# Kernel tuning notes

Hardware: AMD Instinct MI355X
Metric: run time of the kernel (lower is better)

The kernel has to match this reference:

```python
import jax, jax.numpy as jnp
import numpy as np

N = 100000   # nodes
E = 1600000  # edges (avg degree 16)
F = 64       # in_feats
H = 128      # hidden_size
O = 10       # out_feats
L = 3        # SAGEConv layers
EPS = 1e-5


def setup_inputs() -> dict:
    key = jax.random.key(0)
    ks = jax.random.split(key, 16)
    s = 0.05
    return {
        "nodes": jax.random.normal(ks[0], (N, F), jnp.float32),
        "src": jax.random.randint(ks[1], (E,), 0, N),
        "dst": jax.random.randint(ks[2], (E,), 0, N),
        # input MLP: Linear(F,H) -> ReLU -> Linear(H,H)
        "W_in1": jax.random.normal(ks[3], (F, H), jnp.float32) * s,
        "b_in1": jnp.zeros((H,), jnp.float32),
        "W_in2": jax.random.normal(ks[4], (H, H), jnp.float32) * s,
        "b_in2": jnp.zeros((H,), jnp.float32),
        # L stacked SAGEConv layers (mean aggregator)
        "W_self": jax.random.normal(ks[5], (L, H, H), jnp.float32) * s,
        "W_neigh": jax.random.normal(ks[6], (L, H, H), jnp.float32) * s,
        "b_sage": jnp.zeros((L, H), jnp.float32),
        "ln_g": jnp.ones((L, H), jnp.float32),
        "ln_b": jnp.zeros((L, H), jnp.float32),
        # output head Linear(H, O)
        "W_out": jax.random.normal(ks[7], (H, O), jnp.float32) * s,
        "b_out": jnp.zeros((O,), jnp.float32),
    }


def reference(nodes, src, dst, W_in1, b_in1, W_in2, b_in2,
              W_self, W_neigh, b_sage, ln_g, ln_b, W_out, b_out):
    # input MLP
    h = jax.nn.relu(nodes @ W_in1 + b_in1) @ W_in2 + b_in2  # [N, H]

    # in-degree for mean aggregation (0-degree nodes get 0 neighbor feature)
    deg = jax.ops.segment_sum(jnp.ones((E,), h.dtype), dst, num_segments=N)
    inv_deg = (1.0 / jnp.maximum(deg, 1.0))[:, None]  # [N, 1]

    for l in range(L):
        # mean over incoming neighbors: gather src feats, scatter-add to dst
        agg = jax.ops.segment_sum(h[src], dst, num_segments=N) * inv_deg  # [N, H]
        h = h @ W_self[l] + agg @ W_neigh[l] + b_sage[l]
        h = jax.nn.relu(h)
        # LayerNorm over feature dim
        mu = h.mean(-1, keepdims=True)
        var = h.var(-1, keepdims=True)
        h = ln_g[l] * (h - mu) * jax.lax.rsqrt(var + EPS) + ln_b[l]

    # dgl.mean_nodes over the single graph -> [1, H]
    g = h.mean(0, keepdims=True)
    return g @ W_out + b_out  # [1, O]
```

## Files before the change

kernel.cpp:

```cpp
#include <hip/hip_runtime.h>
#include <hip/hip_bf16.h>

#define NN 100000
#define NE 1600000
#define FF 64
#define HH 128
#define OO 10
#define NL 3
#define NB 391
#define NBLK 250
#define CHUNK 6400
#define BCAP 5376
#define LNEPS 1e-5f

typedef short s8v __attribute__((ext_vector_type(8)));
typedef float f32x4 __attribute__((ext_vector_type(4)));
typedef float f32x2 __attribute__((ext_vector_type(2)));

__device__ __forceinline__ unsigned short f2b(float f){
  unsigned u = __float_as_uint(f);
  unsigned r = (u + 0x7FFFu + ((u>>16)&1u)) >> 16;
  return (unsigned short)r;
}
__device__ __forceinline__ float b2f(unsigned short b){
  return __uint_as_float(((unsigned)b)<<16);
}

#if __has_builtin(__builtin_amdgcn_cvt_pk_f32_fp8) && __has_builtin(__builtin_amdgcn_cvt_pk_fp8_f32)
__device__ __forceinline__ unsigned char f8enc(float x){
  int p = __builtin_amdgcn_cvt_pk_fp8_f32(x, x, 0, false);
  return (unsigned char)(p & 0xFF);
}
__device__ __forceinline__ void f8dec4(unsigned u, float* o){
  f32x2 lo = __builtin_amdgcn_cvt_pk_f32_fp8(u, false);
  f32x2 hi = __builtin_amdgcn_cvt_pk_f32_fp8(u, true);
  o[0]=lo[0]; o[1]=lo[1]; o[2]=hi[0]; o[3]=hi[1];
}
#else
#include <hip/hip_fp8.h>
__device__ __forceinline__ unsigned char f8enc(float x){
  __hip_fp8_e4m3 q(x); return (unsigned char)q.__x;
}
__device__ __forceinline__ void f8dec4(unsigned u, float* o){
  for(int i=0;i<4;i++){
    __hip_fp8_e4m3 q; q.__x = (unsigned char)(u>>(8*i));
    o[i] = (float)q;
  }
}
#endif

__global__ __launch_bounds__(256) void k_bcount(const int* __restrict__ dst, int* __restrict__ bcnt,
                                                int* __restrict__ blockcnt){
  __shared__ int h[NB];
  for(int i=threadIdx.x;i<NB;i+=256) h[i]=0;
  __syncthreads();
  int base = blockIdx.x*CHUNK;
  for(int i=threadIdx.x;i<CHUNK;i+=256){
    int e = base+i;
    if(e<NE) atomicAdd(&h[((unsigned)dst[e])>>8],1);
  }
  __syncthreads();
  for(int i=threadIdx.x;i<NB;i+=256){
    int v=h[i];
    blockcnt[i*256 + blockIdx.x] = v;
    if(v) atomicAdd(&bcnt[i],v);
  }
}

__global__ void k_bscan(const int* __restrict__ bcnt, int* __restrict__ boff, int* __restrict__ rowoff){
  __shared__ int s[512];
  int t=threadIdx.x;
  int v = (t<NB)? bcnt[t]:0;
  s[t]=v; __syncthreads();
  for(int off=1;off<512;off<<=1){
    int x=(t>=off)?s[t-off]:0;
    __syncthreads();
    s[t]+=x;
    __syncthreads();
  }
  if(t<NB) boff[t]=s[t]-v;
  if(t==0) rowoff[NN]=NE;
}

__global__ void k_prefix(const int* __restrict__ blockcnt, const int* __restrict__ boff,
                         int* __restrict__ pref){
  __shared__ int s[256];
  int k=blockIdx.x, t=threadIdx.x;
  int v = (t<NBLK)? blockcnt[k*256+t] : 0;
  s[t]=v; __syncthreads();
  for(int off=1;off<256;off<<=1){
    int x=(t>=off)?s[t-off]:0;
    __syncthreads();
    s[t]+=x;
    __syncthreads();
  }
  if(t<NBLK) pref[k*256+t] = boff[k] + s[t]-v;
}

__global__ __launch_bounds__(256) void k_bscatter(const int* __restrict__ src, const int* __restrict__ dst,
                                                  const int* __restrict__ pref, unsigned* __restrict__ ebuf){
  __shared__ int cur[NB];
  __shared__ int pb[NB];
  for(int i=threadIdx.x;i<NB;i+=256){ cur[i]=0; pb[i]=pref[i*256+blockIdx.x]; }
  __syncthreads();
  int base=blockIdx.x*CHUNK;
  for(int i=threadIdx.x;i<CHUNK;i+=256){
    int e=base+i;
    if(e<NE){
      int d=dst[e];
      int k=((unsigned)d)>>8;
      int r=atomicAdd(&cur[k],1);
      ebuf[pb[k]+r] = (unsigned)src[e] | ((unsigned)(d&255)<<20);
    }
  }
}

__global__ __launch_bounds__(256) void k_bsort(const unsigned* __restrict__ ebuf, const int* __restrict__ bcnt,
                                               const int* __restrict__ boff, int* __restrict__ rowoff,
                                               float* __restrict__ invd, int* __restrict__ csr){
  __shared__ unsigned el[BCAP];
  __shared__ int dg[256], sc[256], cu[256];
  int b=blockIdx.x, t=threadIdx.x;
  int c = bcnt[b]; if(c>BCAP) c=BCAP;
  int base = boff[b];
  for(int i=t;i<c;i+=256) el[i]=ebuf[base+i];
  dg[t]=0;
  __syncthreads();
  for(int i=t;i<c;i+=256) atomicAdd(&dg[el[i]>>20],1);
  __syncthreads();
  int v = dg[t];
  sc[t]=v; __syncthreads();
  for(int off=1;off<256;off<<=1){
    int x=(t>=off)?sc[t-off]:0;
    __syncthreads();
    sc[t]+=x;
    __syncthreads();
  }
  int excl = sc[t]-v;
  int node = b*256+t;
  if(node<NN){
    rowoff[node]=base+excl;
    invd[node]=1.0f/fmaxf((float)v,1.0f);
  }
  cu[t]=excl;
  __syncthreads();
  for(int i=t;i<c;i+=256){
    unsigned e=el[i];
    int d=e>>20;
    int p=atomicAdd(&cu[d],1);
    csr[base+p] = (int)(e & 0xFFFFFu);
  }
}

__global__ void k_cvtin(const float* __restrict__ x, unsigned* __restrict__ xb, int n4){
  int i = blockIdx.x*256+threadIdx.x;
  if(i<n4){
    float4 v = *(const float4*)&x[i*4];
    uint2 p;
    p.x = (unsigned)f2b(v.x) | ((unsigned)f2b(v.y)<<16);
    p.y = (unsigned)f2b(v.z) | ((unsigned)f2b(v.w)<<16);
    *(uint2*)&xb[i*2] = p;
  }
}

__global__ void k_repack(const float* __restrict__ W1, const float* __restrict__ W2,
                         const float* __restrict__ Ws, const float* __restrict__ Wn,
                         unsigned short* __restrict__ wf){
  int t = blockIdx.x*256+threadIdx.x;
  if(t >= 122880) return;
  const float* src; int rem;
  if(t < 8192){ src = W1; rem = t; }
  else {
    int u = t - 8192;
    int m = u >> 14; rem = u & 16383;
    if(m==0) src = W2;
    else if(m<=3) src = Ws + (size_t)(m-1)*HH*HH;
    else src = Wn + (size_t)(m-4)*HH*HH;
  }
  int j = rem&7, l=(rem>>3)&63, nt=(rem>>9)&7, kcb=rem>>12;
  int k = kcb*32 + 8*(l>>4) + j;
  int n = nt*16 + (l&15);
  wf[t] = f2b(src[(size_t)k*HH + n]);
}

__global__ __launch_bounds__(256) void k_agg(const uint2* __restrict__ hf8, const int* __restrict__ csr,
                                             const int* __restrict__ rowoff, const float* __restrict__ invd,
                                             uint4* __restrict__ aggb){
  int wave=threadIdx.x>>6, lane=threadIdx.x&63;
  int n = blockIdx.x*4+wave;
  if(n>=NN) return;
  int beg=rowoff[n], end=rowoff[n+1];
  int c = lane&15, q=lane>>4;
  float a0=0.f,a1=0.f,a2=0.f,a3=0.f,a4=0.f,a5=0.f,a6=0.f,a7=0.f;

  int j0 = beg + q;
  int j1 = j0 + 4;
  bool h0 = j0 < end, h1 = j1 < end;
  uint2 u0, u1;
  if(h0) u0 = hf8[(size_t)csr[j0]*16 + c];
  if(h1) u1 = hf8[(size_t)csr[j1]*16 + c];
  while(h0){
    int j2 = j1 + 4;
    bool h2 = j2 < end;
    uint2 u2;
    if(h2) u2 = hf8[(size_t)csr[j2]*16 + c];
    {
      float d0[4], d1[4];
      f8dec4(u0.x,d0); f8dec4(u0.y,d1);
      a0+=d0[0]; a1+=d0[1]; a2+=d0[2]; a3+=d0[3];
      a4+=d1[0]; a5+=d1[1]; a6+=d1[2]; a7+=d1[3];
    }
    u0=u1; h0=h1; j1=j2; u1=u2; h1=h2;
  }

  a0+=__shfl_xor(a0,16); a1+=__shfl_xor(a1,16); a2+=__shfl_xor(a2,16); a3+=__shfl_xor(a3,16);
  a4+=__shfl_xor(a4,16); a5+=__shfl_xor(a5,16); a6+=__shfl_xor(a6,16); a7+=__shfl_xor(a7,16);
  a0+=__shfl_xor(a0,32); a1+=__shfl_xor(a1,32); a2+=__shfl_xor(a2,32); a3+=__shfl_xor(a3,32);
  a4+=__shfl_xor(a4,32); a5+=__shfl_xor(a5,32); a6+=__shfl_xor(a6,32); a7+=__shfl_xor(a7,32);
  if(q==0){
    float s=invd[n];
    uint4 p;
    p.x = (unsigned)f2b(a0*s) | ((unsigned)f2b(a1*s)<<16);
    p.y = (unsigned)f2b(a2*s) | ((unsigned)f2b(a3*s)<<16);
    p.z = (unsigned)f2b(a4*s) | ((unsigned)f2b(a5*s)<<16);
    p.w = (unsigned)f2b(a6*s) | ((unsigned)f2b(a7*s)<<16);
    aggb[(size_t)n*16 + c] = p;
  }
}

template<int K, int DUAL, int RELU, int LN, int F8, int MEAN>
__global__ __launch_bounds__(256) void k_mfma(
    const unsigned short* __restrict__ A, const unsigned short* __restrict__ A2,
    const unsigned short* __restrict__ Wf, const unsigned short* __restrict__ Wf2,
    const float* __restrict__ bias, const float* __restrict__ lng, const float* __restrict__ lnb,
    unsigned short* __restrict__ out, unsigned char* __restrict__ hf8, float* __restrict__ gsum)
{
  constexpr int KC = K/32;
  __shared__ float sm[MEAN ? 4*128 : 4];
  int tid = threadIdx.x;
  int l = tid&63, wv = tid>>6;
  int grp = l>>4, lc = l&15;
  int node0 = blockIdx.x*128;
  const s8v* __restrict__ Wv  = (const s8v*)Wf;
  const s8v* __restrict__ Wv2 = (const s8v*)Wf2;
  f32x4 acc[2][8] = {};
  int r0 = node0 + wv*16 + lc;      if(r0>NN-1) r0=NN-1;
  int r1 = node0 + 64 + wv*16 + lc; if(r1>NN-1) r1=NN-1;
  #pragma unroll
  for(int kcb=0;kcb<KC;kcb++){
    s8v a0 = *(const s8v*)&A[(size_t)r0*K + kcb*32 + 8*grp];
    s8v a1 = *(const s8v*)&A[(size_t)r1*K + kcb*32 + 8*grp];
    s8v c0, c1;
    if(DUAL){
      c0 = *(const s8v*)&A2[(size_t)r0*K + kcb*32 + 8*grp];
      c1 = *(const s8v*)&A2[(size_t)r1*K + kcb*32 + 8*grp];
    }
    #pragma unroll
    for(int nt=0;nt<8;nt++){
      s8v b = Wv[(kcb*8+nt)*64 + l];
      acc[0][nt] = __builtin_amdgcn_mfma_f32_16x16x32_bf16(a0, b, acc[0][nt], 0,0,0);
      acc[1][nt] = __builtin_amdgcn_mfma_f32_16x16x32_bf16(a1, b, acc[1][nt], 0,0,0);
      if(DUAL){
        s8v b2 = Wv2[(kcb*8+nt)*64 + l];
        acc[0][nt] = __builtin_amdgcn_mfma_f32_16x16x32_bf16(c0, b2, acc[0][nt], 0,0,0);
        acc[1][nt] = __builtin_amdgcn_mfma_f32_16x16x32_bf16(c1, b2, acc[1][nt], 0,0,0);
      }
    }
  }
  float bc[8], gc[8], oc[8];
  #pragma unroll
  for(int nt=0;nt<8;nt++){
    bc[nt] = bias[nt*16+lc];
    if(LN){ gc[nt]=lng[nt*16+lc]; oc[nt]=lnb[nt*16+lc]; }
  }
  float msum[8];
  #pragma unroll
  for(int nt=0;nt<8;nt++) msum[nt]=0.f;
  #pragma unroll
  for(int s2=0;s2<2;s2++){
    #pragma unroll
    for(int r=0;r<4;r++){
      float x[8]; float s=0.f, ss=0.f;
      #pragma unroll
      for(int nt=0;nt<8;nt++){
        float v = acc[s2][nt][r] + bc[nt];
        if(RELU) v = fmaxf(v, 0.f);
        x[nt]=v; s+=v; ss+=v*v;
      }
      if(LN){
        #pragma unroll
        for(int m=1;m<=8;m<<=1){ s+=__shfl_xor(s,m); ss+=__shfl_xor(ss,m); }
        float mu = s*(1.0f/HH);
        float var = ss*(1.0f/HH) - mu*mu;
        float rs = rsqrtf(var + LNEPS);
        #pragma unroll
        for(int nt=0;nt<8;nt++) x[nt] = gc[nt]*(x[nt]-mu)*rs + oc[nt];
      }
      int node = node0 + s2*64 + wv*16 + grp*4 + r;
      if(node<NN){
        if(MEAN){
          #pragma unroll
          for(int nt=0;nt<8;nt++) msum[nt]+=x[nt];
        } else {
          #pragma unroll
          for(int nt=0;nt<8;nt++) out[(size_t)node*HH + nt*16 + lc] = f2b(x[nt]);
          if(F8){
            #pragma unroll
            for(int nt=0;nt<8;nt++) hf8[(size_t)node*HH + nt*16 + lc] = f8enc(x[nt]);
          }
        }
      }
    }
  }
  if(MEAN){
    #pragma unroll
    for(int nt=0;nt<8;nt++){
      msum[nt]+=__shfl_xor(msum[nt],16);
      msum[nt]+=__shfl_xor(msum[nt],32);
    }
    if(grp==0){
      #pragma unroll
      for(int nt=0;nt<8;nt++) sm[wv*128 + nt*16 + lc] = msum[nt];
    }
    __syncthreads();
    if(tid<128){
      float v = sm[tid] + sm[128+tid] + sm[256+tid] + sm[384+tid];
      atomicAdd(&gsum[tid], v);
    }
  }
}

__global__ void k_out(const float* __restrict__ g, const float* __restrict__ Wout,
                      const float* __restrict__ bout, float* __restrict__ out){
  int o=threadIdx.x;
  if(o<OO){
    float acc=bout[o];
    for(int k=0;k<HH;k++) acc = fmaf(g[k]*(1.0f/NN), Wout[k*OO+o], acc);
    out[o]=acc;
  }
}

extern "C" void kernel_launch(void* const* d_in, const int* in_sizes, int n_in,
                              void* d_out, int out_size, void* d_ws, size_t ws_size,
                              hipStream_t stream){
  const float* nodes = (const float*)d_in[0];
  const int*   src   = (const int*)d_in[1];
  const int*   dst   = (const int*)d_in[2];
  const float* W_in1 = (const float*)d_in[3];
  const float* b_in1 = (const float*)d_in[4];
  const float* W_in2 = (const float*)d_in[5];
  const float* b_in2 = (const float*)d_in[6];
  const float* W_self  = (const float*)d_in[7];
  const float* W_neigh = (const float*)d_in[8];
  const float* b_sage  = (const float*)d_in[9];
  const float* ln_g    = (const float*)d_in[10];
  const float* ln_b    = (const float*)d_in[11];
  const float* W_out   = (const float*)d_in[12];
  const float* b_out   = (const float*)d_in[13];

  char* w=(char*)d_ws;
  unsigned short* hb   = (unsigned short*)w; w += (size_t)NN*HH*2;
  unsigned short* aggb = (unsigned short*)w; w += (size_t)NN*HH*2;
  unsigned short* xb   = (unsigned short*)w; w += (size_t)NN*FF*2;
  unsigned char*  hf8  = (unsigned char*)w;  w += (size_t)NN*HH;
  unsigned short* wf   = (unsigned short*)w; w += (size_t)122880*2;
  unsigned* ebuf = (unsigned*)w; w += (size_t)NE*4;
  int* csr    = (int*)w;   w += (size_t)NE*4;
  int* rowoff = (int*)w;   w += (size_t)(NN+8)*4;
  float* invd = (float*)w; w += (size_t)NN*4;
  int* bcnt   = (int*)w;   w += (size_t)(NB+1)*4;
  int* boff   = (int*)w;   w += (size_t)(NB+1)*4;
  int* blockcnt=(int*)w;   w += (size_t)NB*256*4;
  int* pref   = (int*)w;   w += (size_t)NB*256*4;
  float* gsum = (float*)w; w += 128*4;

  hipMemsetAsync(bcnt, 0, (size_t)(NB+1)*4, stream);
  hipMemsetAsync(gsum, 0, 128*4, stream);

  k_bcount<<<NBLK,256,0,stream>>>(dst,bcnt,blockcnt);
  k_bscan<<<1,512,0,stream>>>(bcnt,boff,rowoff);
  k_prefix<<<NB,256,0,stream>>>(blockcnt,boff,pref);
  k_bscatter<<<NBLK,256,0,stream>>>(src,dst,pref,ebuf);
  k_bsort<<<NB,256,0,stream>>>(ebuf,bcnt,boff,rowoff,invd,csr);

  k_cvtin<<<((NN*FF/4)+255)/256,256,0,stream>>>(nodes,(unsigned*)xb, NN*FF/4);
  k_repack<<<(122880+255)/256,256,0,stream>>>(W_in1,W_in2,W_self,W_neigh,wf);

  const int GB2 = (NN+127)/128;
  k_mfma<FF,0,1,0,0,0><<<GB2,256,0,stream>>>(xb,nullptr, wf, nullptr, b_in1,nullptr,nullptr, aggb, nullptr, nullptr);
  k_mfma<HH,0,0,0,1,0><<<GB2,256,0,stream>>>(aggb,nullptr, wf+8192, nullptr, b_in2,nullptr,nullptr, hb, hf8, nullptr);

  for(int l=0;l<NL;l++){
    k_agg<<<(NN+3)/4,256,0,stream>>>((const uint2*)hf8,csr,rowoff,invd,(uint4*)aggb);
    if(l<NL-1)
      k_mfma<HH,1,1,1,1,0><<<GB2,256,0,stream>>>(hb, aggb,
          wf+24576+(size_t)l*16384, wf+73728+(size_t)l*16384,
          b_sage+(size_t)l*HH, ln_g+(size_t)l*HH, ln_b+(size_t)l*HH, hb, hf8, nullptr);
    else
      k_mfma<HH,1,1,1,0,1><<<GB2,256,0,stream>>>(hb, aggb,
          wf+24576+(size_t)l*16384, wf+73728+(size_t)l*16384,
          b_sage+(size_t)l*HH, ln_g+(size_t)l*HH, ln_b+(size_t)l*HH, hb, nullptr, gsum);
  }
  k_out<<<1,64,0,stream>>>(gsum,W_out,b_out,(float*)d_out);
}
```

Before: 390.3 us.

## Fuse fp32 input conversion into first GEMM and transpose MFMA output for vector stores

```diff
diff --git a/kernel.cpp b/kernel.cpp
--- a/kernel.cpp
+++ b/kernel.cpp
@@ -22,14 +22,12 @@
   unsigned r = (u + 0x7FFFu + ((u>>16)&1u)) >> 16;
   return (unsigned short)r;
 }
-__device__ __forceinline__ float b2f(unsigned short b){
-  return __uint_as_float(((unsigned)b)<<16);
-}
 
 #if __has_builtin(__builtin_amdgcn_cvt_pk_f32_fp8) && __has_builtin(__builtin_amdgcn_cvt_pk_fp8_f32)
-__device__ __forceinline__ unsigned char f8enc(float x){
-  int p = __builtin_amdgcn_cvt_pk_fp8_f32(x, x, 0, false);
-  return (unsigned char)(p & 0xFF);
+__device__ __forceinline__ unsigned f8pack4(float x0,float x1,float x2,float x3){
+  int p = __builtin_amdgcn_cvt_pk_fp8_f32(x0, x1, 0, false);
+  p = __builtin_amdgcn_cvt_pk_fp8_f32(x2, x3, p, true);
+  return (unsigned)p;
 }
 __device__ __forceinline__ void f8dec4(unsigned u, float* o){
   f32x2 lo = __builtin_amdgcn_cvt_pk_f32_fp8(u, false);
@@ -38,8 +36,9 @@
 }
 #else
 #include <hip/hip_fp8.h>
-__device__ __forceinline__ unsigned char f8enc(float x){
-  __hip_fp8_e4m3 q(x); return (unsigned char)q.__x;
+__device__ __forceinline__ unsigned f8pack4(float x0,float x1,float x2,float x3){
+  __hip_fp8_e4m3 a(x0),b(x1),c(x2),d(x3);
+  return (unsigned)a.__x | ((unsigned)b.__x<<8) | ((unsigned)c.__x<<16) | ((unsigned)d.__x<<24);
 }
 __device__ __forceinline__ void f8dec4(unsigned u, float* o){
   for(int i=0;i<4;i++){
@@ -149,17 +148,6 @@
     int d=e>>20;
     int p=atomicAdd(&cu[d],1);
     csr[base+p] = (int)(e & 0xFFFFFu);
-  }
-}
-
-__global__ void k_cvtin(const float* __restrict__ x, unsigned* __restrict__ xb, int n4){
-  int i = blockIdx.x*256+threadIdx.x;
-  if(i<n4){
-    float4 v = *(const float4*)&x[i*4];
-    uint2 p;
-    p.x = (unsigned)f2b(v.x) | ((unsigned)f2b(v.y)<<16);
-    p.y = (unsigned)f2b(v.z) | ((unsigned)f2b(v.w)<<16);
-    *(uint2*)&xb[i*2] = p;
   }
 }
 
@@ -228,9 +216,9 @@
   }
 }
 
-template<int K, int DUAL, int RELU, int LN, int F8, int MEAN>
+template<int K, int DUAL, int RELU, int LN, int F8, int MEAN, int AF32>
 __global__ __launch_bounds__(256) void k_mfma(
-    const unsigned short* __restrict__ A, const unsigned short* __restrict__ A2,
+    const void* __restrict__ Av, const unsigned short* __restrict__ A2,
     const unsigned short* __restrict__ Wf, const unsigned short* __restrict__ Wf2,
     const float* __restrict__ bias, const float* __restrict__ lng, const float* __restrict__ lnb,
     unsigned short* __restrict__ out, unsigned char* __restrict__ hf8, float* __restrict__ gsum)
@@ -244,70 +232,90 @@
   const s8v* __restrict__ Wv  = (const s8v*)Wf;
   const s8v* __restrict__ Wv2 = (const s8v*)Wf2;
   f32x4 acc[2][8] = {};
-  int r0 = node0 + wv*16 + lc;      if(r0>NN-1) r0=NN-1;
-  int r1 = node0 + 64 + wv*16 + lc; if(r1>NN-1) r1=NN-1;
+  int n0 = node0 + wv*16 + lc;      if(n0>NN-1) n0=NN-1;
+  int n1 = node0 + 64 + wv*16 + lc; if(n1>NN-1) n1=NN-1;
   #pragma unroll
   for(int kcb=0;kcb<KC;kcb++){
-    s8v a0 = *(const s8v*)&A[(size_t)r0*K + kcb*32 + 8*grp];
-    s8v a1 = *(const s8v*)&A[(size_t)r1*K + kcb*32 + 8*grp];
-    s8v c0, c1;
+    s8v b0, b1, d0, d1;
+    if(AF32){
+      const float* Af = (const float*)Av;
+      float4 fa = *(const float4*)&Af[(size_t)n0*K + kcb*32 + 8*grp];
+      float4 fb = *(const float4*)&Af[(size_t)n0*K + kcb*32 + 8*grp + 4];
+      float4 fc = *(const float4*)&Af[(size_t)n1*K + kcb*32 + 8*grp];
+      float4 fd = *(const float4*)&Af[(size_t)n1*K + kcb*32 + 8*grp + 4];
+      b0[0]=(short)f2b(fa.x); b0[1]=(short)f2b(fa.y); b0[2]=(short)f2b(fa.z); b0[3]=(short)f2b(fa.w);
+      b0[4]=(short)f2b(fb.x); b0[5]=(short)f2b(fb.y); b0[6]=(short)f2b(fb.z); b0[7]=(short)f2b(fb.w);
+      b1[0]=(short)f2b(fc.x); b1[1]=(short)f2b(fc.y); b1[2]=(short)f2b(fc.z); b1[3]=(short)f2b(fc.w);
+      b1[4]=(short)f2b(fd.x); b1[5]=(short)f2b(fd.y); b1[6]=(short)f2b(fd.z); b1[7]=(short)f2b(fd.w);
+    } else {
+      const unsigned short* Ab = (const unsigned short*)Av;
+      b0 = *(const s8v*)&Ab[(size_t)n0*K + kcb*32 + 8*grp];
+      b1 = *(const s8v*)&Ab[(size_t)n1*K + kcb*32 + 8*grp];
+    }
     if(DUAL){
-      c0 = *(const s8v*)&A2[(size_t)r0*K + kcb*32 + 8*grp];
-      c1 = *(const s8v*)&A2[(size_t)r1*K + kcb*32 + 8*grp];
+      d0 = *(const s8v*)&A2[(size_t)n0*K + kcb*32 + 8*grp];
+      d1 = *(const s8v*)&A2[(size_t)n1*K + kcb*32 + 8*grp];
     }
     #pragma unroll
     for(int nt=0;nt<8;nt++){
-      s8v b = Wv[(kcb*8+nt)*64 + l];
-      acc[0][nt] = __builtin_amdgcn_mfma_f32_16x16x32_bf16(a0, b, acc[0][nt], 0,0,0);
-      acc[1][nt] = __builtin_amdgcn_mfma_f32_16x16x32_bf16(a1, b, acc[1][nt], 0,0,0);
+      s8v a = Wv[(kcb*8+nt)*64 + l];
+      acc[0][nt] = __builtin_amdgcn_mfma_f32_16x16x32_bf16(a, b0, acc[0][nt], 0,0,0);
+      acc[1][nt] = __builtin_amdgcn_mfma_f32_16x16x32_bf16(a, b1, acc[1][nt], 0,0,0);
       if(DUAL){
-        s8v b2 = Wv2[(kcb*8+nt)*64 + l];
-        acc[0][nt] = __builtin_amdgcn_mfma_f32_16x16x32_bf16(c0, b2, acc[0][nt], 0,0,0);
-        acc[1][nt] = __builtin_amdgcn_mfma_f32_16x16x32_bf16(c1, b2, acc[1][nt], 0,0,0);
+        s8v a2 = Wv2[(kcb*8+nt)*64 + l];
+        acc[0][nt] = __builtin_amdgcn_mfma_f32_16x16x32_bf16(a2, d0, acc[0][nt], 0,0,0);
+        acc[1][nt] = __builtin_amdgcn_mfma_f32_16x16x32_bf16(a2, d1, acc[1][nt], 0,0,0);
       }
     }
   }
-  float bc[8], gc[8], oc[8];
-  #pragma unroll
-  for(int nt=0;nt<8;nt++){
-    bc[nt] = bias[nt*16+lc];
-    if(LN){ gc[nt]=lng[nt*16+lc]; oc[nt]=lnb[nt*16+lc]; }
-  }
-  float msum[8];
-  #pragma unroll
-  for(int nt=0;nt<8;nt++) msum[nt]=0.f;
+  f32x4 msum[MEAN?8:1];
+  if(MEAN){
+    #pragma unroll
+    for(int nt=0;nt<(MEAN?8:1);nt++) msum[nt] = (f32x4){0.f,0.f,0.f,0.f};
+  }
   #pragma unroll
   for(int s2=0;s2<2;s2++){
+    int node = node0 + s2*64 + wv*16 + lc;
+    f32x4 x[8];
+    float s=0.f, ss=0.f;
     #pragma unroll
-    for(int r=0;r<4;r++){
-      float x[8]; float s=0.f, ss=0.f;
+    for(int nt=0;nt<8;nt++){
+      float4 bb = *(const float4*)&bias[nt*16 + grp*4];
+      #pragma unroll
+      for(int r=0;r<4;r++){
+        float v = acc[s2][nt][r] + ((const float*)&bb)[r];
+        if(RELU) v = fmaxf(v, 0.f);
+        x[nt][r]=v; s+=v; ss+=v*v;
+      }
+    }
+    if(LN){
+      s += __shfl_xor(s,16); ss += __shfl_xor(ss,16);
+      s += __shfl_xor(s,32); ss += __shfl_xor(ss,32);
+      float mu = s*(1.0f/HH);
+      float var = ss*(1.0f/HH) - mu*mu;
+      float rs = rsqrtf(var + LNEPS);
       #pragma unroll
       for(int nt=0;nt<8;nt++){
-        float v = acc[s2][nt][r] + bc[nt];
-        if(RELU) v = fmaxf(v, 0.f);
-        x[nt]=v; s+=v; ss+=v*v;
+        float4 gg = *(const float4*)&lng[nt*16 + grp*4];
+        float4 be = *(const float4*)&lnb[nt*16 + grp*4];
+        #pragma unroll
+        for(int r=0;r<4;r++)
+          x[nt][r] = ((const float*)&gg)[r]*(x[nt][r]-mu)*rs + ((const float*)&be)[r];
       }
-      if(LN){
+    }
+    if(node<NN){
+      if(MEAN){
         #pragma unroll
-        for(int m=1;m<=8;m<<=1){ s+=__shfl_xor(s,m); ss+=__shfl_xor(ss,m); }
-        float mu = s*(1.0f/HH);
-        float var = ss*(1.0f/HH) - mu*mu;
-        float rs = rsqrtf(var + LNEPS);
+        for(int nt=0;nt<8;nt++) msum[nt] += x[nt];
+      } else {
         #pragma unroll
-        for(int nt=0;nt<8;nt++) x[nt] = gc[nt]*(x[nt]-mu)*rs + oc[nt];
-      }
-      int node = node0 + s2*64 + wv*16 + grp*4 + r;
-      if(node<NN){
-        if(MEAN){
-          #pragma unroll
-          for(int nt=0;nt<8;nt++) msum[nt]+=x[nt];
-        } else {
-          #pragma unroll
-          for(int nt=0;nt<8;nt++) out[(size_t)node*HH + nt*16 + lc] = f2b(x[nt]);
-          if(F8){
-            #pragma unroll
-            for(int nt=0;nt<8;nt++) hf8[(size_t)node*HH + nt*16 + lc] = f8enc(x[nt]);
-          }
+        for(int nt=0;nt<8;nt++){
+          uint2 pk;
+          pk.x = (unsigned)f2b(x[nt][0]) | ((unsigned)f2b(x[nt][1])<<16);
+          pk.y = (unsigned)f2b(x[nt][2]) | ((unsigned)f2b(x[nt][3])<<16);
+          *(uint2*)&out[(size_t)node*HH + nt*16 + grp*4] = pk;
+          if(F8)
+            *(unsigned*)&hf8[(size_t)node*HH + nt*16 + grp*4] = f8pack4(x[nt][0],x[nt][1],x[nt][2],x[nt][3]);
         }
       }
     }
@@ -315,12 +323,20 @@
   if(MEAN){
     #pragma unroll
     for(int nt=0;nt<8;nt++){
-      msum[nt]+=__shfl_xor(msum[nt],16);
-      msum[nt]+=__shfl_xor(msum[nt],32);
-    }
-    if(grp==0){
       #pragma unroll
-      for(int nt=0;nt<8;nt++) sm[wv*128 + nt*16 + lc] = msum[nt];
+      for(int r=0;r<4;r++){
+        float v = msum[nt][r];
+        v += __shfl_xor(v,1); v += __shfl_xor(v,2);
+        v += __shfl_xor(v,4); v += __shfl_xor(v,8);
+        msum[nt][r]=v;
+      }
+    }
+    if(lc==0){
+      #pragma unroll
+      for(int nt=0;nt<8;nt++)
+        #pragma unroll
+        for(int r=0;r<4;r++)
+          sm[wv*128 + nt*16 + grp*4 + r] = msum[nt][r];
     }
     __syncthreads();
     if(tid<128){
@@ -361,7 +377,6 @@
   char* w=(char*)d_ws;
   unsigned short* hb   = (unsigned short*)w; w += (size_t)NN*HH*2;
   unsigned short* aggb = (unsigned short*)w; w += (size_t)NN*HH*2;
-  unsigned short* xb   = (unsigned short*)w; w += (size_t)NN*FF*2;
   unsigned char*  hf8  = (unsigned char*)w;  w += (size_t)NN*HH;
   unsigned short* wf   = (unsigned short*)w; w += (size_t)122880*2;
   unsigned* ebuf = (unsigned*)w; w += (size_t)NE*4;
@@ -383,21 +398,20 @@
   k_bscatter<<<NBLK,256,0,stream>>>(src,dst,pref,ebuf);
   k_bsort<<<NB,256,0,stream>>>(ebuf,bcnt,boff,rowoff,invd,csr);
 
-  k_cvtin<<<((NN*FF/4)+255)/256,256,0,stream>>>(nodes,(unsigned*)xb, NN*FF/4);
   k_repack<<<(122880+255)/256,256,0,stream>>>(W_in1,W_in2,W_self,W_neigh,wf);
 
   const int GB2 = (NN+127)/128;
-  k_mfma<FF,0,1,0,0,0><<<GB2,256,0,stream>>>(xb,nullptr, wf, nullptr, b_in1,nullptr,nullptr, aggb, nullptr, nullptr);
-  k_mfma<HH,0,0,0,1,0><<<GB2,256,0,stream>>>(aggb,nullptr, wf+8192, nullptr, b_in2,nullptr,nullptr, hb, hf8, nullptr);
+  k_mfma<FF,0,1,0,0,0,1><<<GB2,256,0,stream>>>(nodes,nullptr, wf, nullptr, b_in1,nullptr,nullptr, aggb, nullptr, nullptr);
+  k_mfma<HH,0,0,0,1,0,0><<<GB2,256,0,stream>>>(aggb,nullptr, wf+8192, nullptr, b_in2,nullptr,nullptr, hb, hf8, nullptr);
 
   for(int l=0;l<NL;l++){
     k_agg<<<(NN+3)/4,256,0,stream>>>((const uint2*)hf8,csr,rowoff,invd,(uint4*)aggb);
     if(l<NL-1)
-      k_mfma<HH,1,1,1,1,0><<<GB2,256,0,stream>>>(hb, aggb,
+      k_mfma<HH,1,1,1,1,0,0><<<GB2,256,0,stream>>>(hb, aggb,
           wf+24576+(size_t)l*16384, wf+73728+(size_t)l*16384,
           b_sage+(size_t)l*HH, ln_g+(size_t)l*HH, ln_b+(size_t)l*HH, hb, hf8, nullptr);
     else
-      k_mfma<HH,1,1,1,0,1><<<GB2,256,0,stream>>>(hb, aggb,
+      k_mfma<HH,1,1,1,0,1,0><<<GB2,256,0,stream>>>(hb, aggb,
           wf+24576+(size_t)l*16384, wf+73728+(size_t)l*16384,
           b_sage+(size_t)l*HH, ln_g+(size_t)l*HH, ln_b+(size_t)l*HH, hb, nullptr, gsum);
   }
```

Result: slower. 418.8 us (+7.3%).

## Store fp8 features in column slabs and fuse input bf16 conversion into GEMM

Applied to the files above, without the earlier changes.

```diff
diff --git a/kernel.cpp b/kernel.cpp
--- a/kernel.cpp
+++ b/kernel.cpp
@@ -22,9 +22,6 @@
   unsigned r = (u + 0x7FFFu + ((u>>16)&1u)) >> 16;
   return (unsigned short)r;
 }
-__device__ __forceinline__ float b2f(unsigned short b){
-  return __uint_as_float(((unsigned)b)<<16);
-}
 
 #if __has_builtin(__builtin_amdgcn_cvt_pk_f32_fp8) && __has_builtin(__builtin_amdgcn_cvt_pk_fp8_f32)
 __device__ __forceinline__ unsigned char f8enc(float x){
@@ -149,17 +146,6 @@
     int d=e>>20;
     int p=atomicAdd(&cu[d],1);
     csr[base+p] = (int)(e & 0xFFFFFu);
-  }
-}
-
-__global__ void k_cvtin(const float* __restrict__ x, unsigned* __restrict__ xb, int n4){
-  int i = blockIdx.x*256+threadIdx.x;
-  if(i<n4){
-    float4 v = *(const float4*)&x[i*4];
-    uint2 p;
-    p.x = (unsigned)f2b(v.x) | ((unsigned)f2b(v.y)<<16);
-    p.y = (unsigned)f2b(v.z) | ((unsigned)f2b(v.w)<<16);
-    *(uint2*)&xb[i*2] = p;
   }
 }
 
@@ -183,57 +169,45 @@
   wf[t] = f2b(src[(size_t)k*HH + n]);
 }
 
-__global__ __launch_bounds__(256) void k_agg(const uint2* __restrict__ hf8, const int* __restrict__ csr,
+__global__ __launch_bounds__(256) void k_agg(const unsigned char* __restrict__ hf8T, const int* __restrict__ csr,
                                              const int* __restrict__ rowoff, const float* __restrict__ invd,
-                                             uint4* __restrict__ aggb){
-  int wave=threadIdx.x>>6, lane=threadIdx.x&63;
-  int n = blockIdx.x*4+wave;
+                                             unsigned short* __restrict__ aggs){
+  int b = blockIdx.x;
+  int cb = b & 7;
+  int chunk = b >> 3;
+  int wave = threadIdx.x>>6, lane = threadIdx.x&63;
+  int n = chunk*4 + wave;
   if(n>=NN) return;
   int beg=rowoff[n], end=rowoff[n+1];
-  int c = lane&15, q=lane>>4;
-  float a0=0.f,a1=0.f,a2=0.f,a3=0.f,a4=0.f,a5=0.f,a6=0.f,a7=0.f;
-
-  int j0 = beg + q;
-  int j1 = j0 + 4;
-  bool h0 = j0 < end, h1 = j1 < end;
-  uint2 u0, u1;
-  if(h0) u0 = hf8[(size_t)csr[j0]*16 + c];
-  if(h1) u1 = hf8[(size_t)csr[j1]*16 + c];
-  while(h0){
-    int j2 = j1 + 4;
-    bool h2 = j2 < end;
-    uint2 u2;
-    if(h2) u2 = hf8[(size_t)csr[j2]*16 + c];
-    {
-      float d0[4], d1[4];
-      f8dec4(u0.x,d0); f8dec4(u0.y,d1);
-      a0+=d0[0]; a1+=d0[1]; a2+=d0[2]; a3+=d0[3];
-      a4+=d1[0]; a5+=d1[1]; a6+=d1[2]; a7+=d1[3];
-    }
-    u0=u1; h0=h1; j1=j2; u1=u2; h1=h2;
-  }
-
+  int e = lane>>2, j = lane&3;
+  const unsigned* bse = (const unsigned*)(hf8T + (size_t)cb*NN*16);
+  float a0=0.f,a1=0.f,a2=0.f,a3=0.f;
+  for(int idx=beg+e; idx<end; idx+=16){
+    int s = csr[idx];
+    unsigned u = bse[(size_t)s*4 + j];
+    float d[4];
+    f8dec4(u,d);
+    a0+=d[0]; a1+=d[1]; a2+=d[2]; a3+=d[3];
+  }
+  a0+=__shfl_xor(a0,4);  a1+=__shfl_xor(a1,4);  a2+=__shfl_xor(a2,4);  a3+=__shfl_xor(a3,4);
+  a0+=__shfl_xor(a0,8);  a1+=__shfl_xor(a1,8);  a2+=__shfl_xor(a2,8);  a3+=__shfl_xor(a3,8);
   a0+=__shfl_xor(a0,16); a1+=__shfl_xor(a1,16); a2+=__shfl_xor(a2,16); a3+=__shfl_xor(a3,16);
-  a4+=__shfl_xor(a4,16); a5+=__shfl_xor(a5,16); a6+=__shfl_xor(a6,16); a7+=__shfl_xor(a7,16);
   a0+=__shfl_xor(a0,32); a1+=__shfl_xor(a1,32); a2+=__shfl_xor(a2,32); a3+=__shfl_xor(a3,32);
-  a4+=__shfl_xor(a4,32); a5+=__shfl_xor(a5,32); a6+=__shfl_xor(a6,32); a7+=__shfl_xor(a7,32);
-  if(q==0){
+  if(lane<4){
     float s=invd[n];
-    uint4 p;
+    uint2 p;
     p.x = (unsigned)f2b(a0*s) | ((unsigned)f2b(a1*s)<<16);
     p.y = (unsigned)f2b(a2*s) | ((unsigned)f2b(a3*s)<<16);
-    p.z = (unsigned)f2b(a4*s) | ((unsigned)f2b(a5*s)<<16);
-    p.w = (unsigned)f2b(a6*s) | ((unsigned)f2b(a7*s)<<16);
-    aggb[(size_t)n*16 + c] = p;
-  }
-}
-
-template<int K, int DUAL, int RELU, int LN, int F8, int MEAN>
+    *(uint2*)&aggs[(size_t)cb*NN*16 + (size_t)n*16 + j*4] = p;
+  }
+}
+
+template<int K, int DUAL, int RELU, int LN, int F8, int MEAN, int AF32>
 __global__ __launch_bounds__(256) void k_mfma(
-    const unsigned short* __restrict__ A, const unsigned short* __restrict__ A2,
+    const void* __restrict__ Av, const unsigned short* __restrict__ A2,
     const unsigned short* __restrict__ Wf, const unsigned short* __restrict__ Wf2,
     const float* __restrict__ bias, const float* __restrict__ lng, const float* __restrict__ lnb,
-    unsigned short* __restrict__ out, unsigned char* __restrict__ hf8, float* __restrict__ gsum)
+    unsigned short* __restrict__ out, unsigned char* __restrict__ hf8T, float* __restrict__ gsum)
 {
   constexpr int KC = K/32;
   __shared__ float sm[MEAN ? 4*128 : 4];
@@ -248,12 +222,27 @@
   int r1 = node0 + 64 + wv*16 + lc; if(r1>NN-1) r1=NN-1;
   #pragma unroll
   for(int kcb=0;kcb<KC;kcb++){
-    s8v a0 = *(const s8v*)&A[(size_t)r0*K + kcb*32 + 8*grp];
-    s8v a1 = *(const s8v*)&A[(size_t)r1*K + kcb*32 + 8*grp];
-    s8v c0, c1;
+    int k0 = kcb*32 + 8*grp;
+    s8v a0, a1, c0, c1;
+    if(AF32){
+      const float* Af = (const float*)Av;
+      float4 fa = *(const float4*)&Af[(size_t)r0*K + k0];
+      float4 fb = *(const float4*)&Af[(size_t)r0*K + k0 + 4];
+      float4 fc = *(const float4*)&Af[(size_t)r1*K + k0];
+      float4 fd = *(const float4*)&Af[(size_t)r1*K + k0 + 4];
+      a0[0]=(short)f2b(fa.x); a0[1]=(short)f2b(fa.y); a0[2]=(short)f2b(fa.z); a0[3]=(short)f2b(fa.w);
+      a0[4]=(short)f2b(fb.x); a0[5]=(short)f2b(fb.y); a0[6]=(short)f2b(fb.z); a0[7]=(short)f2b(fb.w);
+      a1[0]=(short)f2b(fc.x); a1[1]=(short)f2b(fc.y); a1[2]=(short)f2b(fc.z); a1[3]=(short)f2b(fc.w);
+      a1[4]=(short)f2b(fd.x); a1[5]=(short)f2b(fd.y); a1[6]=(short)f2b(fd.z); a1[7]=(short)f2b(fd.w);
+    } else {
+      const unsigned short* Ab = (const unsigned short*)Av;
+      a0 = *(const s8v*)&Ab[(size_t)r0*K + k0];
+      a1 = *(const s8v*)&Ab[(size_t)r1*K + k0];
+    }
     if(DUAL){
-      c0 = *(const s8v*)&A2[(size_t)r0*K + kcb*32 + 8*grp];
-      c1 = *(const s8v*)&A2[(size_t)r1*K + kcb*32 + 8*grp];
+      const unsigned short* A2s = A2 + (size_t)(k0>>4)*NN*16 + (k0&15);
+      c0 = *(const s8v*)&A2s[(size_t)r0*16];
+      c1 = *(const s8v*)&A2s[(size_t)r1*16];
     }
     #pragma unroll
     for(int nt=0;nt<8;nt++){
@@ -306,7 +295,7 @@
           for(int nt=0;nt<8;nt++) out[(size_t)node*HH + nt*16 + lc] = f2b(x[nt]);
           if(F8){
             #pragma unroll
-            for(int nt=0;nt<8;nt++) hf8[(size_t)node*HH + nt*16 + lc] = f8enc(x[nt]);
+            for(int nt=0;nt<8;nt++) hf8T[(size_t)nt*NN*16 + (size_t)node*16 + lc] = f8enc(x[nt]);
           }
         }
       }
@@ -360,9 +349,8 @@
 
   char* w=(char*)d_ws;
   unsigned short* hb   = (unsigned short*)w; w += (size_t)NN*HH*2;
-  unsigned short* aggb = (unsigned short*)w; w += (size_t)NN*HH*2;
-  unsigned short* xb   = (unsigned short*)w; w += (size_t)NN*FF*2;
-  unsigned char*  hf8  = (unsigned char*)w;  w += (size_t)NN*HH;
+  unsigned short* aggs = (unsigned short*)w; w += (size_t)NN*HH*2;
+  unsigned char*  hf8T = (unsigned char*)w;  w += (size_t)NN*HH;
   unsigned short* wf   = (unsigned short*)w; w += (size_t)122880*2;
   unsigned* ebuf = (unsigned*)w; w += (size_t)NE*4;
   int* csr    = (int*)w;   w += (size_t)NE*4;
@@ -383,21 +371,21 @@
   k_bscatter<<<NBLK,256,0,stream>>>(src,dst,pref,ebuf);
   k_bsort<<<NB,256,0,stream>>>(ebuf,bcnt,boff,rowoff,invd,csr);
 
-  k_cvtin<<<((NN*FF/4)+255)/256,256,0,stream>>>(nodes,(unsigned*)xb, NN*FF/4);
   k_repack<<<(122880+255)/256,256,0,stream>>>(W_in1,W_in2,W_self,W_neigh,wf);
 
   const int GB2 = (NN+127)/128;
-  k_mfma<FF,0,1,0,0,0><<<GB2,256,0,stream>>>(xb,nullptr, wf, nullptr, b_in1,nullptr,nullptr, aggb, nullptr, nullptr);
-  k_mfma<HH,0,0,0,1,0><<<GB2,256,0,stream>>>(aggb,nullptr, wf+8192, nullptr, b_in2,nullptr,nullptr, hb, hf8, nullptr);
-
+  k_mfma<FF,0,1,0,0,0,1><<<GB2,256,0,stream>>>(nodes,nullptr, wf, nullptr, b_in1,nullptr,nullptr, aggs, nullptr, nullptr);
+  k_mfma<HH,0,0,0,1,0,0><<<GB2,256,0,stream>>>(aggs,nullptr, wf+8192, nullptr, b_in2,nullptr,nullptr, hb, hf8T, nullptr);
+
+  const int GAGG = ((NN+3)/4)*8;
   for(int l=0;l<NL;l++){
-    k_agg<<<(NN+3)/4,256,0,stream>>>((const uint2*)hf8,csr,rowoff,invd,(uint4*)aggb);
+    k_agg<<<GAGG,256,0,stream>>>(hf8T,csr,rowoff,invd,aggs);
     if(l<NL-1)
-      k_mfma<HH,1,1,1,1,0><<<GB2,256,0,stream>>>(hb, aggb,
+      k_mfma<HH,1,1,1,1,0,0><<<GB2,256,0,stream>>>(hb, aggs,
           wf+24576+(size_t)l*16384, wf+73728+(size_t)l*16384,
-          b_sage+(size_t)l*HH, ln_g+(size_t)l*HH, ln_b+(size_t)l*HH, hb, hf8, nullptr);
+          b_sage+(size_t)l*HH, ln_g+(size_t)l*HH, ln_b+(size_t)l*HH, hb, hf8T, nullptr);
     else
-      k_mfma<HH,1,1,1,0,1><<<GB2,256,0,stream>>>(hb, aggb,
+      k_mfma<HH,1,1,1,0,1,0><<<GB2,256,0,stream>>>(hb, aggs,
           wf+24576+(size_t)l*16384, wf+73728+(size_t)l*16384,
           b_sage+(size_t)l*HH, ln_g+(size_t)l*HH, ln_b+(size_t)l*HH, hb, nullptr, gsum);
   }
```

After: 780.5 us. 100.0% more time.
